# Optimization experiments

Hardware: AMD Instinct MI355X
Metric: run time of the kernel (lower is better)

The kernel has to match this reference:

```python
import jax, jax.numpy as jnp
import numpy as np

# Sizes: batch, mapper input dim, subspace dim n, ambient dim k (= n, no equalities),
# number of linear inequalities, number of quadratic constraints.
B, IN_DIM, N, K, M_LIN, QC = 32768, 256, 128, 128, 1024, 16


def setup_inputs() -> dict:
    rng = np.random.default_rng(0)
    x = rng.standard_normal((B, IN_DIM, 1), dtype=np.float32)
    # mapper = nn.Linear(IN_DIM, N)
    W = (rng.standard_normal((N, IN_DIM)) / np.sqrt(IN_DIM)).astype(np.float32)
    b = (0.01 * rng.standard_normal((N,))).astype(np.float32)
    # Linear inequalities A_p z <= b_p, strictly feasible at z0 = 0
    z0 = np.zeros((N, 1), dtype=np.float32)
    A_p = rng.standard_normal((M_LIN, N)).astype(np.float32)
    b_p = (A_p @ z0 + rng.uniform(0.5, 1.5, (M_LIN, 1))).astype(np.float32)
    D = (A_p / (b_p - A_p @ z0)).astype(np.float32)  # D = A_p / ((b_p - A_p z0) 1^T)
    # No equality constraints: y = NA_E z + yp with NA_E = I, yp = 0, y0 = z0
    NA_E = np.eye(K, N, dtype=np.float32)
    yp = np.zeros((K, 1), dtype=np.float32)
    y0 = NA_E @ z0 + yp
    # Quadratic constraints 0.5 y'P y + q'y + r <= 0, strictly feasible at y0.
    # Precompute phi, delta exactly as in ConstraintModule.__init__ (RAYEN branch).
    all_phi = np.empty((QC, 1, K), dtype=np.float32)
    all_delta = np.empty((QC, K, K), dtype=np.float32)
    for i in range(QC):
        G = (rng.standard_normal((K, K)) / np.sqrt(K)).astype(np.float32)
        P = G.T @ G + 0.1 * np.eye(K, dtype=np.float32)
        q = (0.1 * rng.standard_normal((K, 1))).astype(np.float32)
        val0 = 0.5 * y0.T @ P @ y0 + q.T @ y0
        r = -(val0 + np.float32(rng.uniform(0.5, 2.0)))  # value at y0 strictly negative
        quad_at_y0 = 0.5 * y0.T @ P @ y0 + q.T @ y0 + r   # [1,1], < 0
        sigma = 2.0 * quad_at_y0                           # scalar < 0
        g = y0.T @ P + q.T                                 # [1,K]
        all_phi[i] = -g / sigma
        all_delta[i] = (g.T @ g - 4.0 * quad_at_y0 * 0.5 * P) / np.square(sigma)
    return {
        "x": jnp.asarray(x),
        "W": jnp.asarray(W),
        "b": jnp.asarray(b),
        "D": jnp.asarray(D),
        "NA_E": jnp.asarray(NA_E),
        "yp": jnp.asarray(yp),
        "z0": jnp.asarray(z0),
        "all_phi": jnp.asarray(all_phi),
        "all_delta": jnp.asarray(all_delta),
    }


def reference(x, W, b, D, NA_E, yp, z0, all_phi, all_delta):
    Bn = x.shape[0]
    # mapper: x.view(B,-1) -> Linear -> unsqueeze(2)
    v = (x.reshape(Bn, -1) @ W.T + b)[:, :, None]                     # [B,n,1]
    norm_v = jnp.sqrt(jnp.sum(v * v, axis=(1, 2), keepdims=True))    # [B,1,1]
    v_bar = v / jnp.maximum(norm_v, 1e-12)                           # F.normalize
    # kappa from linear constraints: relu(max_m (D v_bar)_m)
    Dv = jnp.einsum('mn,bno->bmo', D, v_bar)                         # [B,M,1]
    kappa = jax.nn.relu(jnp.max(Dv, axis=1, keepdims=True))          # [B,1,1]
    # kappa from quadratic constraints: phi_i rho + sqrt(rho' delta_i rho)
    rho = jnp.einsum('kn,bno->bko', NA_E, v_bar)[..., 0]             # [B,k]
    lin_term = rho @ all_phi[:, 0, :].T                              # [B,Q]
    dr = jnp.einsum('qkl,bl->bqk', all_delta, rho)                   # [B,Q,k]
    quad_term = jnp.einsum('bqk,bk->bq', dr, rho)                    # [B,Q]
    kappa_q = lin_term + jnp.sqrt(quad_term)                         # [B,Q]
    kappa_nl = jnp.max(kappa_q, axis=1)[:, None, None]               # [B,1,1]
    kappa = jnp.maximum(kappa, kappa_nl)
    # alpha = min(1/kappa, ||v||); z = z0 + alpha * v_bar; y = NA_E z + yp
    alpha = jnp.minimum(1.0 / kappa, norm_v)
    z = z0 + alpha * v_bar                                           # [B,n,1]
    y = jnp.einsum('kn,bno->bko', NA_E, z) + yp                      # [B,k,1]
    return y
```

## Files before the change

### kernel.cpp

```cpp
#include <hip/hip_runtime.h>
#include <hip/hip_bf16.h>


typedef __attribute__((ext_vector_type(8))) short short8;
typedef __attribute__((ext_vector_type(4))) float f32x4;
typedef __attribute__((ext_vector_type(4))) unsigned short us4;

__device__ __forceinline__ float bf2f(unsigned short u) {
    union { unsigned int i; float f; } v; v.i = ((unsigned int)u) << 16; return v.f;
}
__device__ __forceinline__ unsigned short f2bf(float f) {
    union { float f; unsigned int i; } v; v.f = f;
    unsigned int r = v.i + 0x7FFFu + ((v.i >> 16) & 1u);
    return (unsigned short)(r >> 16);
}

template<int DT>
__device__ __forceinline__ short8 ld8(const void* p, size_t i) {
    if constexpr (DT == 1) {
        return *reinterpret_cast<const short8*>(reinterpret_cast<const unsigned short*>(p) + i);
    } else {
        const float* f = reinterpret_cast<const float*>(p) + i;
        short8 r;
#pragma unroll
        for (int j = 0; j < 8; ++j) r[j] = (short)f2bf(f[j]);
        return r;
    }
}
template<int DT>
__device__ __forceinline__ float ldf(const void* p, int i) {
    if constexpr (DT == 1) return bf2f(reinterpret_cast<const unsigned short*>(p)[i]);
    else return reinterpret_cast<const float*>(p)[i];
}

__device__ __forceinline__ short8 ld8f4(const float* f) {
    f32x4 a = *reinterpret_cast<const f32x4*>(f);
    f32x4 b = *reinterpret_cast<const f32x4*>(f + 4);
    short8 r;
#pragma unroll
    for (int j = 0; j < 4; ++j) { r[j] = (short)f2bf(a[j]); r[4 + j] = (short)f2bf(b[j]); }
    return r;
}

__device__ __forceinline__ void glds16(const void* g, void* l) {
    __builtin_amdgcn_global_load_lds(
        (const __attribute__((address_space(1))) void*)g,
        (__attribute__((address_space(3))) void*)l, 16, 0, 0);
}

__global__ void detect_dtype(const unsigned short* __restrict__ x, int* __restrict__ flag) {
    __shared__ int cnt;
    if (threadIdx.x == 0) cnt = 0;
    __syncthreads();
    float a = fabsf(bf2f(x[threadIdx.x]));
    int ok = (a > 1e-3f && a < 1e2f) ? 1 : 0;
    atomicAdd(&cnt, ok);
    __syncthreads();
    if (threadIdx.x == 0) *flag = (cnt > 200) ? 1 : 0;
}

__global__ void cvt_const(
    const void* __restrict__ Wp, const void* __restrict__ Dp,
    const void* __restrict__ Qp, const void* __restrict__ Pp,
    unsigned short* __restrict__ Wb, unsigned short* __restrict__ Db,
    unsigned short* __restrict__ Qb, unsigned short* __restrict__ Pb,
    const int* __restrict__ flag)
{
    const int nW = 32768, nD = 131072, nQ = 262144, nP = 2048;
    int idx = blockIdx.x * 256 + threadIdx.x;
    int e = idx * 4;
    if (e >= nW + nD + nQ + nP) return;
    const void* src; unsigned short* dst; int off;
    if      (e < nW)           { src = Wp; dst = Wb; off = e; }
    else if (e < nW + nD)      { src = Dp; dst = Db; off = e - nW; }
    else if (e < nW + nD + nQ) { src = Qp; dst = Qb; off = e - nW - nD; }
    else                       { src = Pp; dst = Pb; off = e - nW - nD - nQ; }
    us4 out;
    if (*flag == 0) {
        f32x4 v = *reinterpret_cast<const f32x4*>(reinterpret_cast<const float*>(src) + off);
#pragma unroll
        for (int j = 0; j < 4; ++j) out[j] = f2bf(v[j]);
    } else {
        out = *reinterpret_cast<const us4*>(reinterpret_cast<const unsigned short*>(src) + off);
    }
    *reinterpret_cast<us4*>(dst + off) = out;
}

template<int DT>
__global__ __launch_bounds__(256, 2) void k1_vbar(
    const void* __restrict__ xp, const unsigned short* __restrict__ Wb,
    const void* __restrict__ bp,
    unsigned short* __restrict__ rho_g, unsigned int* __restrict__ kap_u,
    const int* __restrict__ flag)
{
    if (*flag != DT) return;
    __shared__ unsigned char lds_x[32768];
    __shared__ unsigned char lds_v[16384];
    __shared__ float lds_nsq[64][4];

    const int tid = threadIdx.x;
    const int lane = tid & 63;
    const int w = tid >> 6, hi = lane >> 4, lo = lane & 15;
    const size_t row0 = (size_t)blockIdx.x * 64;

#pragma unroll
    for (int i = 0; i < 8; ++i) {
        int ch = i * 256 + tid;
        int row = ((ch >> 9) << 4) | (ch & 15);
        int off = (((ch >> 6) & 7) << 6) | (((ch >> 4) & 3) << 4);
        if constexpr (DT == 1) {
            glds16((const unsigned char*)xp + (row0 + row) * 512 + off, lds_x + ch * 16);
        } else {
            const float* src = (const float*)xp + (row0 + row) * 256 + (off >> 1);
            *reinterpret_cast<short8*>(lds_x + ch * 16) = ld8f4(src);
        }
    }
    short8 wf[2][8];
#pragma unroll
    for (int ct = 0; ct < 2; ++ct)
#pragma unroll
        for (int kb = 0; kb < 8; ++kb)
            wf[ct][kb] = *reinterpret_cast<const short8*>(
                Wb + (size_t)(w * 32 + ct * 16 + lo) * 256 + kb * 32 + hi * 8);
    if constexpr (DT == 1) { asm volatile("s_waitcnt vmcnt(0)" ::: "memory"); }
    __syncthreads();

    f32x4 acc1[2][4];
#pragma unroll
    for (int c = 0; c < 2; ++c)
#pragma unroll
        for (int r = 0; r < 4; ++r)
#pragma unroll
            for (int e = 0; e < 4; ++e) acc1[c][r][e] = 0.f;
#pragma unroll
    for (int kb = 0; kb < 8; ++kb) {
        short8 af[4];
#pragma unroll
        for (int rt = 0; rt < 4; ++rt)
            af[rt] = *reinterpret_cast<const short8*>(lds_x + (((rt << 3) | kb) << 10) + lane * 16);
#pragma unroll
        for (int ct = 0; ct < 2; ++ct)
#pragma unroll
            for (int rt = 0; rt < 4; ++rt)
                acc1[ct][rt] = __builtin_amdgcn_mfma_f32_16x16x32_bf16(af[rt], wf[ct][kb], acc1[ct][rt], 0, 0, 0);
    }
    float bv[2];
#pragma unroll
    for (int ct = 0; ct < 2; ++ct) bv[ct] = ldf<DT>(bp, w * 32 + ct * 16 + lo);
#pragma unroll
    for (int rt = 0; rt < 4; ++rt)
#pragma unroll
        for (int reg = 0; reg < 4; ++reg) {
            float s = 0.f;
#pragma unroll
            for (int ct = 0; ct < 2; ++ct) {
                float v = acc1[ct][rt][reg] + bv[ct];
                acc1[ct][rt][reg] = v;
                s += v * v;
            }
            s += __shfl_xor(s, 1); s += __shfl_xor(s, 2);
            s += __shfl_xor(s, 4); s += __shfl_xor(s, 8);
            if (lo == 0) lds_nsq[rt * 16 + hi * 4 + reg][w] = s;
        }
    __syncthreads();

#pragma unroll
    for (int rt = 0; rt < 4; ++rt)
#pragma unroll
        for (int reg = 0; reg < 4; ++reg) {
            int row = rt * 16 + hi * 4 + reg;
            float nsq = lds_nsq[row][0] + lds_nsq[row][1] + lds_nsq[row][2] + lds_nsq[row][3];
            float rinv = 1.0f / fmaxf(sqrtf(nsq), 1e-12f);
#pragma unroll
            for (int ct = 0; ct < 2; ++ct) {
                int col = w * 32 + ct * 16 + lo;
                *reinterpret_cast<unsigned short*>(lds_v + row * 256 + col * 2) =
                    f2bf(acc1[ct][rt][reg] * rinv);
            }
        }
    if (tid < 64) {
        float nsq = lds_nsq[tid][0] + lds_nsq[tid][1] + lds_nsq[tid][2] + lds_nsq[tid][3];
        kap_u[row0 + tid] = __float_as_uint(1.0f / sqrtf(nsq));
    }
    __syncthreads();
#pragma unroll
    for (int i = 0; i < 4; ++i) {
        int ch = i * 256 + tid;
        int row = ch >> 4, c16 = ch & 15;
        *reinterpret_cast<short8*>(rho_g + (row0 + row) * 128 + c16 * 8) =
            *reinterpret_cast<const short8*>(lds_v + row * 256 + c16 * 16);
    }
}

__device__ __forceinline__ void stage_rho(const unsigned short* rho_g, size_t row0,
                                          unsigned char* lds_rho, int tid) {
#pragma unroll
    for (int i = 0; i < 4; ++i) {
        int ch = i * 256 + tid;
        int row = ch >> 4;
        int off = (ch & 15) * 16;
        glds16((const unsigned char*)rho_g + (row0 + row) * 256 + (off ^ ((row & 7) << 4)),
               lds_rho + ch * 16);
    }
}

__global__ __launch_bounds__(256, 4) void k2a_dmax(
    const unsigned short* __restrict__ Db, const unsigned short* __restrict__ rho_g,
    unsigned int* __restrict__ kap_u)
{
    __shared__ unsigned char lds_rho[16384];
    __shared__ float lds_red[64][4];
    const int tid = threadIdx.x;
    const int lane = tid & 63;
    const int w = tid >> 6, hi = lane >> 4, lo = lane & 15;
    const size_t row0 = (size_t)blockIdx.x * 64;
    const int mg = blockIdx.y;

    stage_rho(rho_g, row0, lds_rho, tid);
    asm volatile("s_waitcnt vmcnt(0)" ::: "memory");
    __syncthreads();

    short8 af2[4][4];
#pragma unroll
    for (int rt = 0; rt < 4; ++rt)
#pragma unroll
        for (int kb = 0; kb < 4; ++kb) {
            int row = rt * 16 + lo;
            af2[rt][kb] = *reinterpret_cast<const short8*>(
                lds_rho + row * 256 + (((kb << 6) | (hi << 4)) ^ ((lo & 7) << 4)));
        }

    f32x4 dmax[4];
#pragma unroll
    for (int rt = 0; rt < 4; ++rt)
#pragma unroll
        for (int e = 0; e < 4; ++e) dmax[rt][e] = -3e38f;

#pragma unroll 2
    for (int t = 0; t < 4; ++t) {
        int col = mg * 256 + w * 64 + t * 16 + lo;
        short8 bD[4];
#pragma unroll
        for (int kb = 0; kb < 4; ++kb)
            bD[kb] = *reinterpret_cast<const short8*>(Db + (size_t)col * 128 + kb * 32 + hi * 8);
        f32x4 acc[4];
#pragma unroll
        for (int rt = 0; rt < 4; ++rt)
#pragma unroll
            for (int e = 0; e < 4; ++e) acc[rt][e] = 0.f;
#pragma unroll
        for (int kb = 0; kb < 4; ++kb)
#pragma unroll
            for (int rt = 0; rt < 4; ++rt)
                acc[rt] = __builtin_amdgcn_mfma_f32_16x16x32_bf16(af2[rt][kb], bD[kb], acc[rt], 0, 0, 0);
#pragma unroll
        for (int rt = 0; rt < 4; ++rt)
#pragma unroll
            for (int e = 0; e < 4; ++e) dmax[rt][e] = fmaxf(dmax[rt][e], acc[rt][e]);
    }
#pragma unroll
    for (int rt = 0; rt < 4; ++rt)
#pragma unroll
        for (int reg = 0; reg < 4; ++reg) {
            float m = dmax[rt][reg];
            m = fmaxf(m, __shfl_xor(m, 1)); m = fmaxf(m, __shfl_xor(m, 2));
            m = fmaxf(m, __shfl_xor(m, 4)); m = fmaxf(m, __shfl_xor(m, 8));
            if (lo == 0) lds_red[rt * 16 + hi * 4 + reg][w] = m;
        }
    __syncthreads();
    if (tid < 64) {
        float m = fmaxf(fmaxf(lds_red[tid][0], lds_red[tid][1]),
                        fmaxf(lds_red[tid][2], lds_red[tid][3]));
        m = fmaxf(m, 0.f);
        atomicMax(&kap_u[row0 + tid], __float_as_uint(m));
    }
}

__global__ __launch_bounds__(256, 2) void k2b_quad(
    const unsigned short* __restrict__ Qb, const unsigned short* __restrict__ Pb,
    const unsigned short* __restrict__ rho_g, unsigned int* __restrict__ kap_u)
{
    __shared__ unsigned char lds_rho[16384];
    __shared__ float rv_t[128][68];
    const int tid = threadIdx.x;
    const int lane = tid & 63;
    const int w = tid >> 6, hi = lane >> 4, lo = lane & 15;
    const size_t row0 = (size_t)blockIdx.x * 64;
    const int q = blockIdx.y * 4 + w;

    stage_rho(rho_g, row0, lds_rho, tid);
    asm volatile("s_waitcnt vmcnt(0)" ::: "memory");
    __syncthreads();

    {
        int row = tid >> 2;
        int c0 = (tid & 3) * 32;
#pragma unroll
        for (int jb = 0; jb < 4; ++jb) {
            int colbase = c0 + jb * 8;
            short8 v = *reinterpret_cast<const short8*>(
                lds_rho + row * 256 + ((colbase * 2) ^ ((row & 7) << 4)));
#pragma unroll
            for (int j = 0; j < 8; ++j)
                rv_t[colbase + j][row] = bf2f((unsigned short)v[j]);
        }
    }

    short8 af2[4][4];
#pragma unroll
    for (int rt = 0; rt < 4; ++rt)
#pragma unroll
        for (int kb = 0; kb < 4; ++kb) {
            int row = rt * 16 + lo;
            af2[rt][kb] = *reinterpret_cast<const short8*>(
                lds_rho + row * 256 + (((kb << 6) | (hi << 4)) ^ ((lo & 7) << 4)));
        }
    __syncthreads();

    f32x4 accl[4];
#pragma unroll
    for (int rt = 0; rt < 4; ++rt)
#pragma unroll
        for (int e = 0; e < 4; ++e) accl[rt][e] = 0.f;
#pragma unroll
    for (int kb = 0; kb < 4; ++kb) {
        short8 bphi = *reinterpret_cast<const short8*>(
            Pb + (size_t)lo * 128 + kb * 32 + hi * 8);
#pragma unroll
        for (int rt = 0; rt < 4; ++rt)
            accl[rt] = __builtin_amdgcn_mfma_f32_16x16x32_bf16(af2[rt][kb], bphi, accl[rt], 0, 0, 0);
    }

    f32x4 qsum[4];
#pragma unroll
    for (int rt = 0; rt < 4; ++rt)
#pragma unroll
        for (int e = 0; e < 4; ++e) qsum[rt][e] = 0.f;

#pragma unroll 2
    for (int t = 0; t < 8; ++t) {
        int colk = t * 16 + lo;
        short8 bq[4];
#pragma unroll
        for (int kb = 0; kb < 4; ++kb)
            bq[kb] = *reinterpret_cast<const short8*>(
                Qb + ((size_t)q * 128 + colk) * 128 + kb * 32 + hi * 8);
        f32x4 acc[4];
#pragma unroll
        for (int rt = 0; rt < 4; ++rt)
#pragma unroll
            for (int e = 0; e < 4; ++e) acc[rt][e] = 0.f;
#pragma unroll
        for (int kb = 0; kb < 4; ++kb)
#pragma unroll
            for (int rt = 0; rt < 4; ++rt)
                acc[rt] = __builtin_amdgcn_mfma_f32_16x16x32_bf16(af2[rt][kb], bq[kb], acc[rt], 0, 0, 0);
#pragma unroll
        for (int rt = 0; rt < 4; ++rt) {
            f32x4 rv = *reinterpret_cast<const f32x4*>(&rv_t[colk][rt * 16 + hi * 4]);
#pragma unroll
            for (int e = 0; e < 4; ++e)
                qsum[rt][e] += acc[rt][e] * rv[e];
        }
    }
#pragma unroll
    for (int rt = 0; rt < 4; ++rt)
#pragma unroll
        for (int reg = 0; reg < 4; ++reg) {
            float s = qsum[rt][reg];
            s += __shfl_xor(s, 1); s += __shfl_xor(s, 2);
            s += __shfl_xor(s, 4); s += __shfl_xor(s, 8);
            float l = __shfl(accl[rt][reg], hi * 16 + q);
            if (lo == 0) {
                float kq = fmaxf(l + sqrtf(fmaxf(s, 0.f)), 0.f);
                atomicMax(&kap_u[row0 + rt * 16 + hi * 4 + reg], __float_as_uint(kq));
            }
        }
}

template<int DT>
__global__ __launch_bounds__(256, 4) void k3_out(
    const unsigned int* __restrict__ kap_u, const unsigned short* __restrict__ rho_g,
    const void* __restrict__ z0p, const void* __restrict__ ypp,
    void* __restrict__ outp, const int* __restrict__ flag)
{
    if (*flag != DT) return;
    __shared__ float lds_alpha[64];
    const int tid = threadIdx.x;
    const size_t row0 = (size_t)blockIdx.x * 64;

    if (tid < 64)
        lds_alpha[tid] = 1.0f / __uint_as_float(kap_u[row0 + tid]);
    __syncthreads();
#pragma unroll
    for (int i = 0; i < 4; ++i) {
        int idx = tid + i * 256;
        int row = idx >> 4;
        int col0 = (idx & 15) * 8;
        float alpha = lds_alpha[row];
        short8 r8 = *reinterpret_cast<const short8*>(rho_g + (row0 + row) * 128 + col0);
        size_t obase = (row0 + row) * 128 + col0;
        if constexpr (DT == 1) {
            short8 pack;
#pragma unroll
            for (int j = 0; j < 8; ++j) {
                float yv = ldf<1>(z0p, col0 + j) + alpha * bf2f((unsigned short)r8[j])
                         + ldf<1>(ypp, col0 + j);
                pack[j] = (short)f2bf(yv);
            }
            *reinterpret_cast<short8*>(reinterpret_cast<unsigned short*>(outp) + obase) = pack;
        } else {
            f32x4 p0, p1;
#pragma unroll
            for (int j = 0; j < 4; ++j) {
                p0[j] = ldf<0>(z0p, col0 + j) + alpha * bf2f((unsigned short)r8[j])
                      + ldf<0>(ypp, col0 + j);
                p1[j] = ldf<0>(z0p, col0 + 4 + j) + alpha * bf2f((unsigned short)r8[4 + j])
                      + ldf<0>(ypp, col0 + 4 + j);
            }
            *reinterpret_cast<f32x4*>(reinterpret_cast<float*>(outp) + obase) = p0;
            *reinterpret_cast<f32x4*>(reinterpret_cast<float*>(outp) + obase + 4) = p1;
        }
    }
}

template<int DT>
__global__ __launch_bounds__(256, 2) void rayen_mono(
    const void* xp, const void* Wp, const void* bp, const void* Dp,
    const void* ypp, const void* z0p, const void* phip, const void* dltp,
    void* outp, const int* flag)
{
    if (*flag != DT) return;
    __shared__ unsigned char lds_big[49152];
    __shared__ unsigned char lds_rho[16384];
    __shared__ float lds_nsq[64][4];
    __shared__ float lds_dmax[64][4];
    __shared__ float lds_quad[64][16];
    __shared__ float lds_lin[64][16];
    __shared__ float lds_alpha[64];

    const int tid = threadIdx.x;
    const int lane = tid & 63;
    const int w = tid >> 6, hi = lane >> 4, lo = lane & 15;
    const size_t row0 = (size_t)blockIdx.x * 64;
    const unsigned char* Xb = (const unsigned char*)xp;

#pragma unroll
    for (int i = 0; i < 8; ++i) {
        int ch = i * 256 + tid;
        int row = ((ch >> 9) << 4) | (ch & 15);
        int off = (((ch >> 6) & 7) << 6) | (((ch >> 4) & 3) << 4);
        if constexpr (DT == 1)
            glds16(Xb + (row0 + row) * 512 + off, lds_big + ch * 16);
        else {
            const float* src = (const float*)xp + (row0 + row) * 256 + (off >> 1);
            *reinterpret_cast<short8*>(lds_big + ch * 16) = ld8f4(src);
        }
    }
    short8 wf[2][8];
#pragma unroll
    for (int ct = 0; ct < 2; ++ct)
#pragma unroll
        for (int kb = 0; kb < 8; ++kb)
            wf[ct][kb] = ld8<DT>(Wp, (size_t)(w * 32 + ct * 16 + lo) * 256 + kb * 32 + hi * 8);
    asm volatile("s_waitcnt vmcnt(0)" ::: "memory");
    __syncthreads();

    f32x4 acc1[2][4];
#pragma unroll
    for (int c = 0; c < 2; ++c)
#pragma unroll
        for (int r = 0; r < 4; ++r)
#pragma unroll
            for (int e = 0; e < 4; ++e) acc1[c][r][e] = 0.f;
#pragma unroll
    for (int kb = 0; kb < 8; ++kb) {
        short8 af[4];
#pragma unroll
        for (int rt = 0; rt < 4; ++rt)
            af[rt] = *reinterpret_cast<const short8*>(lds_big + (((rt << 3) | kb) << 10) + lane * 16);
#pragma unroll
        for (int ct = 0; ct < 2; ++ct)
#pragma unroll
            for (int rt = 0; rt < 4; ++rt)
                acc1[ct][rt] = __builtin_amdgcn_mfma_f32_16x16x32_bf16(af[rt], wf[ct][kb], acc1[ct][rt], 0, 0, 0);
    }
    float bv[2];
#pragma unroll
    for (int ct = 0; ct < 2; ++ct) bv[ct] = ldf<DT>(bp, w * 32 + ct * 16 + lo);
#pragma unroll
    for (int rt = 0; rt < 4; ++rt)
#pragma unroll
        for (int reg = 0; reg < 4; ++reg) {
            float s = 0.f;
#pragma unroll
            for (int ct = 0; ct < 2; ++ct) {
                float v = acc1[ct][rt][reg] + bv[ct];
                acc1[ct][rt][reg] = v;
                s += v * v;
            }
            s += __shfl_xor(s, 1); s += __shfl_xor(s, 2);
            s += __shfl_xor(s, 4); s += __shfl_xor(s, 8);
            if (lo == 0) lds_nsq[rt * 16 + hi * 4 + reg][w] = s;
        }
    __syncthreads();
#pragma unroll
    for (int rt = 0; rt < 4; ++rt)
#pragma unroll
        for (int reg = 0; reg < 4; ++reg) {
            int row = rt * 16 + hi * 4 + reg;
            float nsq = lds_nsq[row][0] + lds_nsq[row][1] + lds_nsq[row][2] + lds_nsq[row][3];
            float rinv = 1.0f / fmaxf(sqrtf(nsq), 1e-12f);
#pragma unroll
            for (int ct = 0; ct < 2; ++ct) {
                int col = w * 32 + ct * 16 + lo;
                *reinterpret_cast<unsigned short*>(
                    lds_rho + row * 256 + ((col * 2) ^ ((row & 7) << 4))) =
                    f2bf(acc1[ct][rt][reg] * rinv);
            }
        }
    __syncthreads();
    short8 af2[4][4];
#pragma unroll
    for (int rt = 0; rt < 4; ++rt)
#pragma unroll
        for (int kb = 0; kb < 4; ++kb) {
            int row = rt * 16 + lo;
            af2[rt][kb] = *reinterpret_cast<const short8*>(
                lds_rho + row * 256 + (((kb << 6) | (hi << 4)) ^ ((lo & 7) << 4)));
        }
    unsigned char* wbase = lds_big + w * 12288;
    auto stage_q = [&](int p, int b) {
        unsigned char* dst0 = wbase + b * 4096;
#pragma unroll
        for (int kb = 0; kb < 4; ++kb) {
            size_t grow; const void* base;
            if (p < 16) { base = Dp; grow = (size_t)(p * 64 + w * 16 + lo); }
            else {
                int pd = p - 16;
                base = dltp;
                grow = (size_t)((((pd >> 3) * 4 + w) * 128) + ((pd & 7) * 16 + lo));
            }
            if constexpr (DT == 1)
                glds16((const unsigned char*)base + grow * 256 + kb * 64 + hi * 16, dst0 + kb * 1024);
            else {
                const float* src = (const float*)base + grow * 128 + kb * 32 + hi * 8;
                *reinterpret_cast<short8*>(dst0 + kb * 1024 + lane * 16) = ld8f4(src);
            }
        }
    };
    f32x4 dmax[4], qsum[4];
#pragma unroll
    for (int rt = 0; rt < 4; ++rt)
#pragma unroll
        for (int e = 0; e < 4; ++e) { dmax[rt][e] = -3e38f; qsum[rt][e] = 0.f; }
    stage_q(0, 0); stage_q(1, 1);
#pragma unroll 1
    for (int p = 0; p < 48; ++p) {
        if constexpr (DT == 1) {
            if (p < 47) { asm volatile("s_waitcnt vmcnt(4)" ::: "memory"); }
            else        { asm volatile("s_waitcnt vmcnt(0)" ::: "memory"); }
        } else {
            asm volatile("s_waitcnt vmcnt(0) lgkmcnt(0)" ::: "memory");
        }
        __builtin_amdgcn_sched_barrier(0);
        if (p + 2 < 48) stage_q(p + 2, (p + 2) % 3);
        unsigned char* buf = wbase + (p % 3) * 4096;
        f32x4 acc[4];
#pragma unroll
        for (int rt = 0; rt < 4; ++rt)
#pragma unroll
            for (int e = 0; e < 4; ++e) acc[rt][e] = 0.f;
#pragma unroll
        for (int kb = 0; kb < 4; ++kb) {
            short8 bf = *reinterpret_cast<const short8*>(buf + kb * 1024 + lane * 16);
#pragma unroll
            for (int rt = 0; rt < 4; ++rt)
                acc[rt] = __builtin_amdgcn_mfma_f32_16x16x32_bf16(af2[rt][kb], bf, acc[rt], 0, 0, 0);
        }
        if (p < 16) {
#pragma unroll
            for (int rt = 0; rt < 4; ++rt)
#pragma unroll
                for (int e = 0; e < 4; ++e) dmax[rt][e] = fmaxf(dmax[rt][e], acc[rt][e]);
        } else {
            int pd = p - 16, kr = (pd & 7) << 4;
#pragma unroll
            for (int rt = 0; rt < 4; ++rt)
#pragma unroll
                for (int e = 0; e < 4; ++e) {
                    int row = rt * 16 + hi * 4 + e;
                    float rvv = bf2f(*reinterpret_cast<const unsigned short*>(
                        lds_rho + row * 256 + ((((kr + lo) * 2)) ^ ((row & 7) << 4))));
                    qsum[rt][e] += acc[rt][e] * rvv;
                }
            if ((pd & 7) == 7) {
#pragma unroll
                for (int rt = 0; rt < 4; ++rt)
#pragma unroll
                    for (int e = 0; e < 4; ++e) {
                        float s = qsum[rt][e];
                        s += __shfl_xor(s, 1); s += __shfl_xor(s, 2);
                        s += __shfl_xor(s, 4); s += __shfl_xor(s, 8);
                        if (lo == 0) lds_quad[rt * 16 + hi * 4 + e][((pd >> 3) << 2) | w] = s;
                        qsum[rt][e] = 0.f;
                    }
            }
        }
    }
#pragma unroll
    for (int rt = 0; rt < 4; ++rt)
#pragma unroll
        for (int reg = 0; reg < 4; ++reg) {
            float m = dmax[rt][reg];
            m = fmaxf(m, __shfl_xor(m, 1)); m = fmaxf(m, __shfl_xor(m, 2));
            m = fmaxf(m, __shfl_xor(m, 4)); m = fmaxf(m, __shfl_xor(m, 8));
            if (lo == 0) lds_dmax[rt * 16 + hi * 4 + reg][w] = m;
        }
    if (w == 0) {
        f32x4 accp[4];
#pragma unroll
        for (int rt = 0; rt < 4; ++rt)
#pragma unroll
            for (int e = 0; e < 4; ++e) accp[rt][e] = 0.f;
#pragma unroll
        for (int kb = 0; kb < 4; ++kb) {
            short8 bp8 = ld8<DT>(phip, (size_t)lo * 128 + kb * 32 + hi * 8);
#pragma unroll
            for (int rt = 0; rt < 4; ++rt)
                accp[rt] = __builtin_amdgcn_mfma_f32_16x16x32_bf16(af2[rt][kb], bp8, accp[rt], 0, 0, 0);
        }
#pragma unroll
        for (int rt = 0; rt < 4; ++rt)
#pragma unroll
            for (int reg = 0; reg < 4; ++reg)
                lds_lin[rt * 16 + hi * 4 + reg][lo] = accp[rt][reg];
    }
    __syncthreads();
    if (tid < 64) {
        int row = tid;
        float nsq = lds_nsq[row][0] + lds_nsq[row][1] + lds_nsq[row][2] + lds_nsq[row][3];
        float norm = sqrtf(nsq);
        float kap = fmaxf(0.f, fmaxf(fmaxf(lds_dmax[row][0], lds_dmax[row][1]),
                                     fmaxf(lds_dmax[row][2], lds_dmax[row][3])));
#pragma unroll
        for (int q = 0; q < 16; ++q)
            kap = fmaxf(kap, lds_lin[row][q] + sqrtf(fmaxf(lds_quad[row][q], 0.f)));
        lds_alpha[row] = fminf(1.0f / kap, norm);
    }
    __syncthreads();
#pragma unroll
    for (int i = 0; i < 4; ++i) {
        int idx = tid + i * 256;
        int row = idx >> 4, col0 = (idx & 15) * 8;
        float alpha = lds_alpha[row];
        short8 r8 = *reinterpret_cast<const short8*>(
            lds_rho + row * 256 + ((col0 * 2) ^ ((row & 7) << 4)));
        float yv[8];
#pragma unroll
        for (int j = 0; j < 8; ++j)
            yv[j] = ldf<DT>(z0p, col0 + j) + alpha * bf2f((unsigned short)r8[j]) + ldf<DT>(ypp, col0 + j);
        size_t obase = (row0 + row) * 128 + col0;
        if constexpr (DT == 1) {
            short8 pack;
#pragma unroll
            for (int j = 0; j < 8; ++j) pack[j] = (short)f2bf(yv[j]);
            *reinterpret_cast<short8*>(reinterpret_cast<unsigned short*>(outp) + obase) = pack;
        } else {
            f32x4 p0, p1;
#pragma unroll
            for (int j = 0; j < 4; ++j) { p0[j] = yv[j]; p1[j] = yv[4 + j]; }
            *reinterpret_cast<f32x4*>(reinterpret_cast<float*>(outp) + obase) = p0;
            *reinterpret_cast<f32x4*>(reinterpret_cast<float*>(outp) + obase + 4) = p1;
        }
    }
}

extern "C" void kernel_launch(void* const* d_in, const int* in_sizes, int n_in,
                              void* d_out, int out_size, void* d_ws, size_t ws_size,
                              hipStream_t stream) {
    const void* x    = d_in[0];
    const void* W    = d_in[1];
    const void* b    = d_in[2];
    const void* D    = d_in[3];
    const void* yp   = d_in[5];
    const void* z0   = d_in[6];
    const void* phi  = d_in[7];
    const void* dlt  = d_in[8];

    const int B = in_sizes[0] / 256;
    const int tiles = B / 64;

    unsigned char* ws = reinterpret_cast<unsigned char*>(d_ws);
    int* flag = reinterpret_cast<int*>(ws);
    unsigned int*   kap_u = reinterpret_cast<unsigned int*>(ws + 4096);
    unsigned short* Wb    = reinterpret_cast<unsigned short*>(ws + 135168);
    unsigned short* Db    = reinterpret_cast<unsigned short*>(ws + 200704);
    unsigned short* Qb    = reinterpret_cast<unsigned short*>(ws + 462848);
    unsigned short* Pb    = reinterpret_cast<unsigned short*>(ws + 987136);
    unsigned short* rho_g = reinterpret_cast<unsigned short*>(ws + 991232);
    const size_t need = 991232 + (size_t)B * 256;

    detect_dtype<<<dim3(1), dim3(256), 0, stream>>>(
        reinterpret_cast<const unsigned short*>(x), flag);

    dim3 blk(256);
    if (ws_size >= need) {
        cvt_const<<<dim3((428032 / 4 + 255) / 256), blk, 0, stream>>>(
            W, D, dlt, phi, Wb, Db, Qb, Pb, flag);
        k1_vbar<0><<<dim3(tiles), blk, 0, stream>>>(x, Wb, b, rho_g, kap_u, flag);
        k1_vbar<1><<<dim3(tiles), blk, 0, stream>>>(x, Wb, b, rho_g, kap_u, flag);
        k2a_dmax<<<dim3(tiles, 4), blk, 0, stream>>>(Db, rho_g, kap_u);
        k2b_quad<<<dim3(tiles, 4), blk, 0, stream>>>(Qb, Pb, rho_g, kap_u);
        k3_out<0><<<dim3(tiles), blk, 0, stream>>>(kap_u, rho_g, z0, yp, d_out, flag);
        k3_out<1><<<dim3(tiles), blk, 0, stream>>>(kap_u, rho_g, z0, yp, d_out, flag);
    } else {
        rayen_mono<1><<<dim3(tiles), blk, 0, stream>>>(x, W, b, D, yp, z0, phi, dlt, d_out, flag);
        rayen_mono<0><<<dim3(tiles), blk, 0, stream>>>(x, W, b, D, yp, z0, phi, dlt, d_out, flag);
    }
}
```

Baseline: 108.7 us.

## Restructure quadratic kernel to keep one delta matrix in LDS across row tiles

The quadratic-constraint kernel is reorganised so each block owns one constraint q. It stages that q's 128x128 bf16 delta matrix into LDS once, then loops over 16 row tiles, double-buffering the rho tiles. The intent is to stop re-reading delta from global/L2 for every 64-row tile. In the new layout all four waves of a block compute the same q over the same rows, so MFMA and atomic work is duplicated fourfold. The rho values are also now read as individual bf16 scalars from LDS. Separately, the fp32 W and phi loads are switched to vectorized float4 loads, and bf16 rounding now uses the HIP intrinsic.

```diff
diff --git a/kernel.cpp b/kernel.cpp
--- a/kernel.cpp
+++ b/kernel.cpp
@@ -10,23 +10,10 @@
     union { unsigned int i; float f; } v; v.i = ((unsigned int)u) << 16; return v.f;
 }
 __device__ __forceinline__ unsigned short f2bf(float f) {
-    union { float f; unsigned int i; } v; v.f = f;
-    unsigned int r = v.i + 0x7FFFu + ((v.i >> 16) & 1u);
-    return (unsigned short)(r >> 16);
-}
-
-template<int DT>
-__device__ __forceinline__ short8 ld8(const void* p, size_t i) {
-    if constexpr (DT == 1) {
-        return *reinterpret_cast<const short8*>(reinterpret_cast<const unsigned short*>(p) + i);
-    } else {
-        const float* f = reinterpret_cast<const float*>(p) + i;
-        short8 r;
-#pragma unroll
-        for (int j = 0; j < 8; ++j) r[j] = (short)f2bf(f[j]);
-        return r;
-    }
-}
+    __hip_bfloat16 h = __float2bfloat16(f);
+    return *reinterpret_cast<unsigned short*>(&h);
+}
+
 template<int DT>
 __device__ __forceinline__ float ldf(const void* p, int i) {
     if constexpr (DT == 1) return bf2f(reinterpret_cast<const unsigned short*>(p)[i]);
@@ -276,106 +263,114 @@
     }
 }
 
-__global__ __launch_bounds__(256, 2) void k2b_quad(
+__global__ __launch_bounds__(256, 2) void k2b_ws(
     const unsigned short* __restrict__ Qb, const unsigned short* __restrict__ Pb,
     const unsigned short* __restrict__ rho_g, unsigned int* __restrict__ kap_u)
 {
-    __shared__ unsigned char lds_rho[16384];
-    __shared__ float rv_t[128][68];
+    __shared__ unsigned char lds_dlt[32768];
+    __shared__ unsigned char lds_rho0[16384];
+    __shared__ unsigned char lds_rho1[16384];
     const int tid = threadIdx.x;
     const int lane = tid & 63;
     const int w = tid >> 6, hi = lane >> 4, lo = lane & 15;
-    const size_t row0 = (size_t)blockIdx.x * 64;
-    const int q = blockIdx.y * 4 + w;
-
-    stage_rho(rho_g, row0, lds_rho, tid);
+    const int q = blockIdx.y;
+    const int g0 = blockIdx.x * 16;
+
+#pragma unroll
+    for (int i = 0; i < 8; ++i) {
+        int ch = i * 256 + tid;
+        int f = ch >> 6, l = ch & 63;
+        int t = f >> 2, kb = f & 3;
+        size_t elem = ((size_t)q * 128 + t * 16 + (l & 15)) * 128 + kb * 32 + (l >> 4) * 8;
+        glds16((const unsigned char*)Qb + elem * 2, lds_dlt + ch * 16);
+    }
+    stage_rho(rho_g, (size_t)g0 * 64, lds_rho0, tid);
     asm volatile("s_waitcnt vmcnt(0)" ::: "memory");
     __syncthreads();
 
-    {
-        int row = tid >> 2;
-        int c0 = (tid & 3) * 32;
-#pragma unroll
-        for (int jb = 0; jb < 4; ++jb) {
-            int colbase = c0 + jb * 8;
-            short8 v = *reinterpret_cast<const short8*>(
-                lds_rho + row * 256 + ((colbase * 2) ^ ((row & 7) << 4)));
-#pragma unroll
-            for (int j = 0; j < 8; ++j)
-                rv_t[colbase + j][row] = bf2f((unsigned short)v[j]);
-        }
-    }
-
-    short8 af2[4][4];
-#pragma unroll
-    for (int rt = 0; rt < 4; ++rt)
+#pragma unroll 1
+    for (int g = 0; g < 16; ++g) {
+        unsigned char* rb = (g & 1) ? lds_rho1 : lds_rho0;
+        unsigned char* nb = (g & 1) ? lds_rho0 : lds_rho1;
+        const size_t row0 = (size_t)(g0 + g) * 64;
+
+        if (g + 1 < 16)
+            stage_rho(rho_g, (size_t)(g0 + g + 1) * 64, nb, tid);
+
+        short8 af2[4][4];
+#pragma unroll
+        for (int rt = 0; rt < 4; ++rt)
+#pragma unroll
+            for (int kb = 0; kb < 4; ++kb) {
+                int row = rt * 16 + lo;
+                af2[rt][kb] = *reinterpret_cast<const short8*>(
+                    rb + row * 256 + (((kb << 6) | (hi << 4)) ^ ((lo & 7) << 4)));
+            }
+
+        f32x4 accl[4];
+#pragma unroll
+        for (int rt = 0; rt < 4; ++rt)
+#pragma unroll
+            for (int e = 0; e < 4; ++e) accl[rt][e] = 0.f;
 #pragma unroll
         for (int kb = 0; kb < 4; ++kb) {
-            int row = rt * 16 + lo;
-            af2[rt][kb] = *reinterpret_cast<const short8*>(
-                lds_rho + row * 256 + (((kb << 6) | (hi << 4)) ^ ((lo & 7) << 4)));
-        }
-    __syncthreads();
-
-    f32x4 accl[4];
-#pragma unroll
-    for (int rt = 0; rt < 4; ++rt)
-#pragma unroll
-        for (int e = 0; e < 4; ++e) accl[rt][e] = 0.f;
-#pragma unroll
-    for (int kb = 0; kb < 4; ++kb) {
-        short8 bphi = *reinterpret_cast<const short8*>(
-            Pb + (size_t)lo * 128 + kb * 32 + hi * 8);
-#pragma unroll
-        for (int rt = 0; rt < 4; ++rt)
-            accl[rt] = __builtin_amdgcn_mfma_f32_16x16x32_bf16(af2[rt][kb], bphi, accl[rt], 0, 0, 0);
-    }
-
-    f32x4 qsum[4];
-#pragma unroll
-    for (int rt = 0; rt < 4; ++rt)
-#pragma unroll
-        for (int e = 0; e < 4; ++e) qsum[rt][e] = 0.f;
+            short8 bphi = *reinterpret_cast<const short8*>(
+                Pb + (size_t)lo * 128 + kb * 32 + hi * 8);
+#pragma unroll
+            for (int rt = 0; rt < 4; ++rt)
+                accl[rt] = __builtin_amdgcn_mfma_f32_16x16x32_bf16(af2[rt][kb], bphi, accl[rt], 0, 0, 0);
+        }
+
+        f32x4 qsum[4];
+#pragma unroll
+        for (int rt = 0; rt < 4; ++rt)
+#pragma unroll
+            for (int e = 0; e < 4; ++e) qsum[rt][e] = 0.f;
 
 #pragma unroll 2
-    for (int t = 0; t < 8; ++t) {
-        int colk = t * 16 + lo;
-        short8 bq[4];
-#pragma unroll
-        for (int kb = 0; kb < 4; ++kb)
-            bq[kb] = *reinterpret_cast<const short8*>(
-                Qb + ((size_t)q * 128 + colk) * 128 + kb * 32 + hi * 8);
-        f32x4 acc[4];
-#pragma unroll
-        for (int rt = 0; rt < 4; ++rt)
-#pragma unroll
-            for (int e = 0; e < 4; ++e) acc[rt][e] = 0.f;
-#pragma unroll
-        for (int kb = 0; kb < 4; ++kb)
-#pragma unroll
-            for (int rt = 0; rt < 4; ++rt)
-                acc[rt] = __builtin_amdgcn_mfma_f32_16x16x32_bf16(af2[rt][kb], bq[kb], acc[rt], 0, 0, 0);
-#pragma unroll
-        for (int rt = 0; rt < 4; ++rt) {
-            f32x4 rv = *reinterpret_cast<const f32x4*>(&rv_t[colk][rt * 16 + hi * 4]);
-#pragma unroll
-            for (int e = 0; e < 4; ++e)
-                qsum[rt][e] += acc[rt][e] * rv[e];
-        }
-    }
-#pragma unroll
-    for (int rt = 0; rt < 4; ++rt)
-#pragma unroll
-        for (int reg = 0; reg < 4; ++reg) {
-            float s = qsum[rt][reg];
-            s += __shfl_xor(s, 1); s += __shfl_xor(s, 2);
-            s += __shfl_xor(s, 4); s += __shfl_xor(s, 8);
-            float l = __shfl(accl[rt][reg], hi * 16 + q);
-            if (lo == 0) {
-                float kq = fmaxf(l + sqrtf(fmaxf(s, 0.f)), 0.f);
-                atomicMax(&kap_u[row0 + rt * 16 + hi * 4 + reg], __float_as_uint(kq));
-            }
-        }
+        for (int t = 0; t < 8; ++t) {
+            int colk = t * 16 + lo;
+            short8 bq[4];
+#pragma unroll
+            for (int kb = 0; kb < 4; ++kb)
+                bq[kb] = *reinterpret_cast<const short8*>(
+                    lds_dlt + (((t << 2) | kb) << 10) + lane * 16);
+            f32x4 acc[4];
+#pragma unroll
+            for (int rt = 0; rt < 4; ++rt)
+#pragma unroll
+                for (int e = 0; e < 4; ++e) acc[rt][e] = 0.f;
+#pragma unroll
+            for (int kb = 0; kb < 4; ++kb)
+#pragma unroll
+                for (int rt = 0; rt < 4; ++rt)
+                    acc[rt] = __builtin_amdgcn_mfma_f32_16x16x32_bf16(af2[rt][kb], bq[kb], acc[rt], 0, 0, 0);
+#pragma unroll
+            for (int rt = 0; rt < 4; ++rt)
+#pragma unroll
+                for (int e = 0; e < 4; ++e) {
+                    int row = rt * 16 + hi * 4 + e;
+                    float rv = bf2f(*reinterpret_cast<const unsigned short*>(
+                        rb + row * 256 + ((colk * 2) ^ ((row & 7) << 4))));
+                    qsum[rt][e] += acc[rt][e] * rv;
+                }
+        }
+#pragma unroll
+        for (int rt = 0; rt < 4; ++rt)
+#pragma unroll
+            for (int reg = 0; reg < 4; ++reg) {
+                float s = qsum[rt][reg];
+                s += __shfl_xor(s, 1); s += __shfl_xor(s, 2);
+                s += __shfl_xor(s, 4); s += __shfl_xor(s, 8);
+                float l = __shfl(accl[rt][reg], hi * 16 + q);
+                if (lo == 0) {
+                    float kq = fmaxf(l + sqrtf(fmaxf(s, 0.f)), 0.f);
+                    atomicMax(&kap_u[row0 + rt * 16 + hi * 4 + reg], __float_as_uint(kq));
+                }
+            }
+        asm volatile("s_waitcnt vmcnt(0)" ::: "memory");
+        __syncthreads();
+    }
 }
 
 template<int DT>
@@ -461,8 +456,13 @@
 #pragma unroll
     for (int ct = 0; ct < 2; ++ct)
 #pragma unroll
-        for (int kb = 0; kb < 8; ++kb)
-            wf[ct][kb] = ld8<DT>(Wp, (size_t)(w * 32 + ct * 16 + lo) * 256 + kb * 32 + hi * 8);
+        for (int kb = 0; kb < 8; ++kb) {
+            if constexpr (DT == 1)
+                wf[ct][kb] = *reinterpret_cast<const short8*>(
+                    (const unsigned short*)Wp + (size_t)(w * 32 + ct * 16 + lo) * 256 + kb * 32 + hi * 8);
+            else
+                wf[ct][kb] = ld8f4((const float*)Wp + (size_t)(w * 32 + ct * 16 + lo) * 256 + kb * 32 + hi * 8);
+        }
     asm volatile("s_waitcnt vmcnt(0)" ::: "memory");
     __syncthreads();
 
@@ -625,7 +625,12 @@
             for (int e = 0; e < 4; ++e) accp[rt][e] = 0.f;
 #pragma unroll
         for (int kb = 0; kb < 4; ++kb) {
-            short8 bp8 = ld8<DT>(phip, (size_t)lo * 128 + kb * 32 + hi * 8);
+            short8 bp8;
+            if constexpr (DT == 1)
+                bp8 = *reinterpret_cast<const short8*>(
+                    (const unsigned short*)phip + (size_t)lo * 128 + kb * 32 + hi * 8);
+            else
+                bp8 = ld8f4((const float*)phip + (size_t)lo * 128 + kb * 32 + hi * 8);
 #pragma unroll
             for (int rt = 0; rt < 4; ++rt)
                 accp[rt] = __builtin_amdgcn_mfma_f32_16x16x32_bf16(af2[rt][kb], bp8, accp[rt], 0, 0, 0);
@@ -711,7 +716,7 @@
         k1_vbar<0><<<dim3(tiles), blk, 0, stream>>>(x, Wb, b, rho_g, kap_u, flag);
         k1_vbar<1><<<dim3(tiles), blk, 0, stream>>>(x, Wb, b, rho_g, kap_u, flag);
         k2a_dmax<<<dim3(tiles, 4), blk, 0, stream>>>(Db, rho_g, kap_u);
-        k2b_quad<<<dim3(tiles, 4), blk, 0, stream>>>(Qb, Pb, rho_g, kap_u);
+        k2b_ws<<<dim3(tiles / 16, 16), blk, 0, stream>>>(Qb, Pb, rho_g, kap_u);
         k3_out<0><<<dim3(tiles), blk, 0, stream>>>(kap_u, rho_g, z0, yp, d_out, flag);
         k3_out<1><<<dim3(tiles), blk, 0, stream>>>(kap_u, rho_g, z0, yp, d_out, flag);
     } else {
```

Result: slower. 212.3 us (+95.3%).
